# Performance work log

Measured on AMD Instinct MI355X. Metric: run time of the kernel, lower is better.

## Reference

```python
import jax, jax.numpy as jnp
import numpy as np

D_MODEL = 768
N_HEADS = 8
HEAD_DIM = D_MODEL // N_HEADS  # 96


def setup_inputs() -> dict:
    key = jax.random.key(0)
    k1, k2, k3, k4, k5 = jax.random.split(key, 5)
    B, LQ, LK = 2, 4096, 4096
    hidden_states = jax.random.normal(k1, (B, LQ, D_MODEL), dtype=jnp.float32)
    key_value_states = jax.random.normal(k2, (B, LK, D_MODEL), dtype=jnp.float32)
    # learned projection params (initialized as eye in torch, but learned; use random here)
    Wq = jax.random.normal(k3, (D_MODEL, D_MODEL), dtype=jnp.float32) * 0.02
    Wk = jax.random.normal(k4, (D_MODEL, D_MODEL), dtype=jnp.float32) * 0.02
    Wv = jax.random.normal(k5, (D_MODEL, D_MODEL), dtype=jnp.float32) * 0.02
    return {"hidden_states": hidden_states, "key_value_states": key_value_states,
            "Wq": Wq, "Wk": Wk, "Wv": Wv}


def reference(hidden_states, key_value_states, Wq, Wk, Wv):
    B, LQ, _ = hidden_states.shape
    LK = key_value_states.shape[1]
    # linear projections (no bias)
    q = hidden_states @ Wq            # [B, LQ, D]
    k = key_value_states @ Wk         # [B, LK, D]
    v = key_value_states @ Wv         # [B, LK, D]
    # split heads: [B, H, L, d]
    def shape(x, L):
        return x.reshape(B, L, N_HEADS, HEAD_DIM).transpose(0, 2, 1, 3)
    q = shape(q, LQ) / jnp.sqrt(jnp.float32(HEAD_DIM))
    k = shape(k, LK)
    v = shape(v, LK)
    scores = jnp.einsum('bhqd,bhkd->bhqk', q, k)   # [B, H, LQ, LK]
    attn = jax.nn.softmax(scores, axis=-1)
    # dropout p=0.0 -> identity
    ctx = jnp.einsum('bhqk,bhkd->bhqd', attn, v)   # [B, H, LQ, d]
    context = ctx.transpose(0, 2, 1, 3).reshape(B, LQ, D_MODEL)
    return context
```

## Files before the change

kernel.cpp:

```cpp
#include <hip/hip_runtime.h>
#include <hip/hip_bf16.h>


typedef __bf16 bf16x8 __attribute__((ext_vector_type(8)));
typedef __bf16 bf16x4 __attribute__((ext_vector_type(4)));
typedef float  f32x4  __attribute__((ext_vector_type(4)));
typedef float  f32x16 __attribute__((ext_vector_type(16)));
typedef unsigned u32x4 __attribute__((ext_vector_type(4)));

#define DM   768
#define NH   8
#define HD   96
#define SEQ  4096
#define BATCH 2
#define WELEM (DM*DM)
#define XELEM (BATCH*SEQ*DM)

#define GLDS16(gp, lp) __builtin_amdgcn_global_load_lds( \
    (const __attribute__((address_space(1))) void*)(gp), \
    (__attribute__((address_space(3))) void*)(lp), 16, 0, 0)

__global__ __launch_bounds__(256) void prep(
    const float* __restrict__ hidden, const float* __restrict__ kv,
    const float* __restrict__ Wq, const float* __restrict__ Wk,
    const float* __restrict__ Wv,
    __bf16* __restrict__ Xh_bf, __bf16* __restrict__ Xkv_bf,
    __bf16* __restrict__ Tq, __bf16* __restrict__ Tk, __bf16* __restrict__ Tv)
{
    __shared__ __bf16 Ls[64][72];
    const int id = blockIdx.x;
    const int t = threadIdx.x;

    if (id < 6144) {
        const int half = id >= 3072;
        const float* X = half ? kv : hidden;
        __bf16* Y      = half ? Xkv_bf : Xh_bf;
        const size_t i = ((size_t)(id - half * 3072) * 256 + t) * 8;
        float4 lo = *reinterpret_cast<const float4*>(X + i);
        float4 hi = *reinterpret_cast<const float4*>(X + i + 4);
        bf16x8 v;
        v[0]=(__bf16)lo.x; v[1]=(__bf16)lo.y; v[2]=(__bf16)lo.z; v[3]=(__bf16)lo.w;
        v[4]=(__bf16)hi.x; v[5]=(__bf16)hi.y; v[6]=(__bf16)hi.z; v[7]=(__bf16)hi.w;
        *reinterpret_cast<bf16x8*>(Y + i) = v;
        return;
    }

    const int id2 = id - 6144;
    const int which = id2 / 144;
    const int tile = id2 - which * 144;
    const int ti = tile / 12, tj = tile % 12;
    const float* W = (which == 0) ? Wq : (which == 1) ? Wk : Wv;
    __bf16* T      = (which == 0) ? Tq : (which == 1) ? Tk : Tv;

    const int row = t >> 2, q4 = t & 3;
    const float* src = W + (size_t)(ti * 64 + row) * DM + tj * 64 + q4 * 16;
    float4 f0 = *reinterpret_cast<const float4*>(src);
    float4 f1 = *reinterpret_cast<const float4*>(src + 4);
    float4 f2 = *reinterpret_cast<const float4*>(src + 8);
    float4 f3 = *reinterpret_cast<const float4*>(src + 12);
    bf16x8 v0, v1;
    v0[0]=(__bf16)f0.x; v0[1]=(__bf16)f0.y; v0[2]=(__bf16)f0.z; v0[3]=(__bf16)f0.w;
    v0[4]=(__bf16)f1.x; v0[5]=(__bf16)f1.y; v0[6]=(__bf16)f1.z; v0[7]=(__bf16)f1.w;
    v1[0]=(__bf16)f2.x; v1[1]=(__bf16)f2.y; v1[2]=(__bf16)f2.z; v1[3]=(__bf16)f2.w;
    v1[4]=(__bf16)f3.x; v1[5]=(__bf16)f3.y; v1[6]=(__bf16)f3.z; v1[7]=(__bf16)f3.w;
    *reinterpret_cast<bf16x8*>(&Ls[row][q4 * 16])     = v0;
    *reinterpret_cast<bf16x8*>(&Ls[row][q4 * 16 + 8]) = v1;
    __syncthreads();
    #pragma unroll
    for (int j = 0; j < 2; ++j) {
        const int idx = t + j * 256;
        const int orow = idx >> 3, oc = idx & 7;
        bf16x8 o;
        #pragma unroll
        for (int e = 0; e < 8; ++e) o[e] = Ls[oc * 8 + e][orow];
        *reinterpret_cast<bf16x8*>(
            &T[(size_t)(tj * 64 + orow) * DM + ti * 64 + oc * 8]) = o;
    }
}

__global__ __launch_bounds__(256, 2) void proj_all(
    const __bf16* __restrict__ Xh, const __bf16* __restrict__ Xkv,
    const __bf16* __restrict__ Wtq, const __bf16* __restrict__ Wtk,
    const __bf16* __restrict__ Wtv, __bf16* __restrict__ Yq,
    __bf16* __restrict__ Yk, __bf16* __restrict__ Yv, float qscale)
{
    __shared__ __bf16 As[2][128][64];
    __shared__ __bf16 Bs[2][128][64];

    const int t = threadIdx.x;
    const int l = t & 63;
    const int w = t >> 6;
    const int ln = l & 15, g = l >> 4;
    const int wm = w >> 1, wn = w & 1;

    const int id3 = blockIdx.x;
    const int xcd = id3 & 7;
    const int u = id3 >> 3;
    const int which = u % 3;
    const int c = u / 3;
    const int m0 = (xcd * 8 + c / 6) * 128;
    const int n0 = (c % 6) * 128;

    const __bf16* Xb = (which == 0) ? Xh : Xkv;
    const __bf16* Wt = (which == 0) ? Wtq : (which == 1) ? Wtk : Wtv;
    __bf16* Y        = (which == 0) ? Yq : (which == 1) ? Yk : Yv;
    const int mode   = (which == 2) ? 1 : 0;
    const float scale = (which == 0) ? qscale : 1.0f;

    size_t asrc[4], bsrc[4]; unsigned sdst[4];
    #pragma unroll
    for (int j = 0; j < 4; ++j) {
        const int cid = j * 256 + t;
        const int r = cid >> 3, cc = cid & 7, cs = cc ^ (r & 7);
        asrc[j] = (size_t)(m0 + r) * DM + cs * 8;
        bsrc[j] = (size_t)(n0 + r) * DM + cs * 8;
        sdst[j] = cid * 16;
    }

    f32x4 acc[4][4] = {};

    #pragma unroll
    for (int j = 0; j < 4; ++j) GLDS16(Xb + asrc[j], (char*)As + sdst[j]);
    #pragma unroll
    for (int j = 0; j < 4; ++j) GLDS16(Wt + bsrc[j], (char*)Bs + sdst[j]);
    __syncthreads();

    const int NKT = DM / 64;
    for (int kt = 0; kt < NKT; ++kt) {
        const int cur = kt & 1;
        if (kt + 1 < NKT) {
            const unsigned nb = (cur ^ 1) * 16384u;
            const size_t k0n = (size_t)(kt + 1) * 64;
            #pragma unroll
            for (int j = 0; j < 4; ++j) GLDS16(Xb + k0n + asrc[j], (char*)As + nb + sdst[j]);
            #pragma unroll
            for (int j = 0; j < 4; ++j) GLDS16(Wt + k0n + bsrc[j], (char*)Bs + nb + sdst[j]);
        }

        #pragma unroll
        for (int kk = 0; kk < 2; ++kk) {
            bf16x8 a[4], b[4];
            #pragma unroll
            for (int ms = 0; ms < 4; ++ms) {
                const int row = wm * 64 + ms * 16 + ln;
                const int slot = (kk * 4 + g) ^ (row & 7);
                a[ms] = *reinterpret_cast<const bf16x8*>(
                    (const char*)As + cur * 16384 + row * 128 + slot * 16);
            }
            #pragma unroll
            for (int ns = 0; ns < 4; ++ns) {
                const int row = wn * 64 + ns * 16 + ln;
                const int slot = (kk * 4 + g) ^ (row & 7);
                b[ns] = *reinterpret_cast<const bf16x8*>(
                    (const char*)Bs + cur * 16384 + row * 128 + slot * 16);
            }
            #pragma unroll
            for (int ms = 0; ms < 4; ++ms)
                #pragma unroll
                for (int ns = 0; ns < 4; ++ns)
                    acc[ms][ns] = __builtin_amdgcn_mfma_f32_16x16x32_bf16(
                        a[ms], b[ns], acc[ms][ns], 0, 0, 0);
        }
        __syncthreads();
    }

    #pragma unroll
    for (int ms = 0; ms < 4; ++ms) {
        #pragma unroll
        for (int ns = 0; ns < 4; ++ns) {
            const int col = n0 + wn * 64 + ns * 16 + ln;
            const int h = col / HD, d = col - h * HD;
            const int row_base = m0 + wm * 64 + ms * 16 + 4 * g;
            if (mode == 0) {
                #pragma unroll
                for (int r = 0; r < 4; ++r) {
                    const int row = row_base + r;
                    const int b_ = row >> 12, q = row & (SEQ - 1);
                    Y[(((size_t)(b_ * NH + h) * SEQ) + q) * HD + d] =
                        (__bf16)(acc[ms][ns][r] * scale);
                }
            } else {
                const int b_ = row_base >> 12, kq = row_base & (SEQ - 1);
                bf16x4 v;
                #pragma unroll
                for (int r = 0; r < 4; ++r) v[r] = (__bf16)acc[ms][ns][r];
                *reinterpret_cast<bf16x4*>(
                    &Y[((size_t)(b_ * NH + h) * HD + d) * SEQ + kq]) = v;
            }
        }
    }
}

__global__ __launch_bounds__(512, 2) void attn_kernel(
    const __bf16* __restrict__ Q, const __bf16* __restrict__ K,
    const __bf16* __restrict__ Vt, float* __restrict__ out)
{
    __shared__ __bf16 Ks[2][64][128];
    __shared__ __bf16 Vs[2][96][64];

    const int t_ = threadIdx.x;
    const int l = t_ & 63;
    const int w = t_ >> 6;
    const int lh = l >> 5;
    const int c31 = l & 31;
    const int ord = (w >> 2) & 1;

    const int swz = (blockIdx.x & 7) * 32 + (blockIdx.x >> 3);
    const int bh = swz >> 4;
    const int qb = swz & 15;
    const int b = bh >> 3, hd = bh & 7;
    const int q0 = qb * 256 + w * 32;

    const size_t base = (size_t)bh * SEQ * HD;
    const __bf16* Kg = K + base;
    const __bf16* Vg = Vt + base;

    size_t ksrc[2], vsrc[2];
    unsigned kdst[2], vdst[2];
    #pragma unroll
    for (int j = 0; j < 2; ++j) {
        const int cid = j * 512 + t_;
        const int r = cid >> 4, cc = cid & 15;
        int cs = cc ^ (r & 7); if (cs >= 12) cs = 0;
        ksrc[j] = (size_t)r * HD + cs * 8;
        kdst[j] = cid * 16;
        const int vid = j * 512 + t_;
        const int d = vid >> 3, cc2 = vid & 7;
        const int cs2 = cc2 ^ (d & 7);
        vsrc[j] = (size_t)(d < 96 ? d : 0) * SEQ + cs2 * 8;
        vdst[j] = vid * 16;
    }
    const bool vdo2 = t_ < 256;

    bf16x8 qf[6];
    #pragma unroll
    for (int st = 0; st < 6; ++st)
        qf[st] = *reinterpret_cast<const bf16x8*>(
            &Q[base + (size_t)(q0 + c31) * HD + st * 16 + 8 * lh]);

    const char* kb[6];
    #pragma unroll
    for (int st = 0; st < 6; ++st)
        kb[st] = (const char*)Ks + c31 * 256 + (((2 * st + lh) ^ (c31 & 7)) * 16);
    const char* vp[4];
    #pragma unroll
    for (int kc = 0; kc < 4; ++kc)
        vp[kc] = (const char*)Vs + c31 * 128 + (((2 * kc + lh) ^ (c31 & 7)) * 16);

    f32x16 acc[3] = {};
    f32x16 sA0, sA1, sB0, sB1;
    float l_r = 0.f;

    auto STAGE_K = [&](int tile, int kp) {
        const size_t ko = (size_t)tile * 64 * HD;
        #pragma unroll
        for (int j = 0; j < 2; ++j)
            GLDS16(Kg + ko + ksrc[j], (char*)Ks + kp * 16384 + kdst[j]);
    };
    auto STAGE_V = [&](int tile, int vbuf) {
        const size_t vo = (size_t)tile * 64;
        GLDS16(Vg + vo + vsrc[0], (char*)Vs + vbuf * 12288 + vdst[0]);
        if (vdo2)
            GLDS16(Vg + vo + vsrc[1], (char*)Vs + vbuf * 12288 + vdst[1]);
    };

    auto QKT = [&](const int pbuf, f32x16& S0, f32x16& S1) {
        S0 = (f32x16){}; S1 = (f32x16){};
        #pragma unroll
        for (int st = 0; st < 6; ++st) {
            bf16x8 ka0 = *reinterpret_cast<const bf16x8*>(kb[st] + pbuf * 16384);
            bf16x8 ka1 = *reinterpret_cast<const bf16x8*>(kb[st] + pbuf * 16384 + 8192);
            S0 = __builtin_amdgcn_mfma_f32_32x32x16_bf16(ka0, qf[st], S0, 0, 0, 0);
            S1 = __builtin_amdgcn_mfma_f32_32x32x16_bf16(ka1, qf[st], S1, 0, 0, 0);
        }
    };

    auto SMPV = [&](const int vbuf, f32x16& S0, f32x16& S1) {
        float p0 = 0.f, p1 = 0.f;
        #pragma unroll
        for (int r = 0; r < 16; ++r) {
            const float e0 = __builtin_amdgcn_exp2f(S0[r]);
            const float e1 = __builtin_amdgcn_exp2f(S1[r]);
            S0[r] = e0; S1[r] = e1; p0 += e0; p1 += e1;
        }
        l_r += p0 + p1;
        unsigned up[2][4][2];
        #pragma unroll
        for (int qd = 0; qd < 4; ++qd)
            #pragma unroll
            for (int j = 0; j < 2; ++j) {
                asm("v_cvt_pk_bf16_f32 %0, %1, %2"
                    : "=v"(up[0][qd][j])
                    : "v"(S0[4 * qd + 2 * j]), "v"(S0[4 * qd + 2 * j + 1]));
                asm("v_cvt_pk_bf16_f32 %0, %1, %2"
                    : "=v"(up[1][qd][j])
                    : "v"(S1[4 * qd + 2 * j]), "v"(S1[4 * qd + 2 * j + 1]));
            }
        #pragma unroll
        for (int kc = 0; kc < 4; ++kc) {
            const int ks = kc >> 1, cp = kc & 1;
            unsigned x0 = up[ks][2 * cp][0],     x1 = up[ks][2 * cp][1];
            unsigned y0 = up[ks][2 * cp + 1][0], y1 = up[ks][2 * cp + 1][1];
            asm("v_permlane32_swap_b32 %0, %1" : "+v"(x0), "+v"(y0));
            asm("v_permlane32_swap_b32 %0, %1" : "+v"(x1), "+v"(y1));
            u32x4 pw; pw[0] = x0; pw[1] = x1; pw[2] = y0; pw[3] = y1;
            const bf16x8 pa = __builtin_bit_cast(bf16x8, pw);
            __builtin_amdgcn_s_setprio(1);
            #pragma unroll
            for (int dt = 0; dt < 3; ++dt) {
                bf16x8 vb = *reinterpret_cast<const bf16x8*>(
                    vp[kc] + vbuf * 12288 + dt * 4096);
                acc[dt] = __builtin_amdgcn_mfma_f32_32x32x16_bf16(pa, vb, acc[dt], 0, 0, 0);
            }
            __builtin_amdgcn_s_setprio(0);
        }
    };

    STAGE_K(0, 0);
    STAGE_V(0, 0);
    __syncthreads();
    STAGE_K(1, 1);
    QKT(0, sA0, sA1);

    const int NT = SEQ / 64;
    if (ord == 0) {
        for (int u2 = 0; u2 < NT / 2; ++u2) {
            const int u = 2 * u2;
            __syncthreads();
            if (u + 2 < NT) STAGE_K(u + 2, 0);
            STAGE_V(u + 1, 1);
            QKT(1, sB0, sB1);
            SMPV(0, sA0, sA1);
            __syncthreads();
            if (u + 3 < NT) STAGE_K(u + 3, 1);
            if (u + 2 < NT) STAGE_V(u + 2, 0);
            if (u + 2 < NT) QKT(0, sA0, sA1);
            SMPV(1, sB0, sB1);
        }
    } else {
        for (int u2 = 0; u2 < NT / 2; ++u2) {
            const int u = 2 * u2;
            __syncthreads();
            if (u + 2 < NT) STAGE_K(u + 2, 0);
            STAGE_V(u + 1, 1);
            SMPV(0, sA0, sA1);
            QKT(1, sB0, sB1);
            __syncthreads();
            if (u + 3 < NT) STAGE_K(u + 3, 1);
            if (u + 2 < NT) STAGE_V(u + 2, 0);
            SMPV(1, sB0, sB1);
            if (u + 2 < NT) QKT(0, sA0, sA1);
        }
    }

    {
        float ex = l_r;
        asm volatile("" : "+v"(ex));
        asm("v_permlane32_swap_b32 %0, %1" : "+v"(ex), "+v"(l_r));
        l_r += ex;
    }
    const float inv = 1.0f / l_r;
    #pragma unroll
    for (int r = 0; r < 16; ++r) {
        const int ql = (r & 3) + 8 * (r >> 2) + 4 * lh;
        const float ir = __shfl(inv, ql, 64);
        const int q = q0 + ql;
        float* dst = out + ((size_t)(b * SEQ + q)) * DM + hd * HD;
        #pragma unroll
        for (int dt = 0; dt < 3; ++dt)
            dst[dt * 32 + c31] = acc[dt][r] * ir;
    }
}

extern "C" void kernel_launch(void* const* d_in, const int* in_sizes, int n_in,
                              void* d_out, int out_size, void* d_ws, size_t ws_size,
                              hipStream_t stream) {
    const float* hidden = (const float*)d_in[0];
    const float* kv     = (const float*)d_in[1];
    const float* Wq     = (const float*)d_in[2];
    const float* Wk     = (const float*)d_in[3];
    const float* Wv     = (const float*)d_in[4];
    float* out = (float*)d_out;

    __bf16* Wt_q = (__bf16*)d_ws;
    __bf16* Wt_k = Wt_q + WELEM;
    __bf16* Wt_v = Wt_k + WELEM;
    __bf16* Qb   = Wt_v + WELEM;
    __bf16* Kb   = Qb + XELEM;
    __bf16* Vtb  = Kb + XELEM;

    __bf16* Xh_bf  = (__bf16*)d_out;
    __bf16* Xkv_bf = Xh_bf + XELEM;

    prep<<<6576, 256, 0, stream>>>(hidden, kv, Wq, Wk, Wv,
                                   Xh_bf, Xkv_bf, Wt_q, Wt_k, Wt_v);

    const float qscale = 0.10206207261596575f * 1.4426950408889634f;
    proj_all<<<1152, 256, 0, stream>>>(Xh_bf, Xkv_bf, Wt_q, Wt_k, Wt_v,
                                       Qb, Kb, Vtb, qscale);

    attn_kernel<<<256, 512, 0, stream>>>(Qb, Kb, Vtb, out);
}
```

Baseline: 169.5 us.

## Split attention over key halves and combine partial results in a second kernel

The attention kernel now splits the key sequence into two halves, and each block handles 512 queries (64 per wave, two 32-row MFMA tiles) against one 2048-key half. K and V tiles shrink to 32 keys, so each K fragment read from LDS feeds two MFMAs. Each block writes unnormalized fp32 partial contexts and row sums to the output or a scratch buffer. A new combine kernel adds the two partials and divides by the summed row totals. This raises register use and LDS reuse per wave, at the cost of writing and re-reading a full fp32 context buffer plus an extra launch. The softmax has no running max, so adding the two unnormalized halves stays exact.

```diff
diff --git a/kernel.cpp b/kernel.cpp
--- a/kernel.cpp
+++ b/kernel.cpp
@@ -191,12 +191,13 @@
     }
 }
 
-__global__ __launch_bounds__(512, 2) void attn_kernel(
+__global__ __launch_bounds__(512, 2) void attn_split(
     const __bf16* __restrict__ Q, const __bf16* __restrict__ K,
-    const __bf16* __restrict__ Vt, float* __restrict__ out)
+    const __bf16* __restrict__ Vt, float* __restrict__ ctx0,
+    float* __restrict__ ctx1, float* __restrict__ lsum)
 {
-    __shared__ __bf16 Ks[2][64][128];
-    __shared__ __bf16 Vs[2][96][64];
+    __shared__ __bf16 Ks[2][32][128];
+    __shared__ __bf16 Vs[2][96][32];
 
     const int t_ = threadIdx.x;
     const int l = t_ & 63;
@@ -207,71 +208,63 @@
 
     const int swz = (blockIdx.x & 7) * 32 + (blockIdx.x >> 3);
     const int bh = swz >> 4;
-    const int qb = swz & 15;
+    const int rem = swz & 15;
+    const int kh = rem >> 3;
+    const int qbb = rem & 7;
     const int b = bh >> 3, hd = bh & 7;
-    const int q0 = qb * 256 + w * 32;
+    const int q0 = qbb * 512 + w * 64;
 
     const size_t base = (size_t)bh * SEQ * HD;
-    const __bf16* Kg = K + base;
-    const __bf16* Vg = Vt + base;
-
-    size_t ksrc[2], vsrc[2];
-    unsigned kdst[2], vdst[2];
-    #pragma unroll
-    for (int j = 0; j < 2; ++j) {
-        const int cid = j * 512 + t_;
-        const int r = cid >> 4, cc = cid & 15;
-        int cs = cc ^ (r & 7); if (cs >= 12) cs = 0;
-        ksrc[j] = (size_t)r * HD + cs * 8;
-        kdst[j] = cid * 16;
-        const int vid = j * 512 + t_;
-        const int d = vid >> 3, cc2 = vid & 7;
-        const int cs2 = cc2 ^ (d & 7);
-        vsrc[j] = (size_t)(d < 96 ? d : 0) * SEQ + cs2 * 8;
-        vdst[j] = vid * 16;
-    }
-    const bool vdo2 = t_ < 256;
-
-    bf16x8 qf[6];
-    #pragma unroll
-    for (int st = 0; st < 6; ++st)
-        qf[st] = *reinterpret_cast<const bf16x8*>(
-            &Q[base + (size_t)(q0 + c31) * HD + st * 16 + 8 * lh]);
+    const __bf16* Kg = K + base + (size_t)kh * 2048 * HD;
+    const __bf16* Vg = Vt + base + (size_t)kh * 2048;
+
+    const int kr = t_ >> 4, kcc = t_ & 15;
+    int kcs = kcc ^ (kr & 7); if (kcs >= 12) kcs = 0;
+    const size_t ksrc = (size_t)kr * HD + kcs * 8;
+    const unsigned kdst = t_ * 16;
+    const int vd = t_ >> 2, vcc = t_ & 3;
+    const int vcs = (vcc - (vd >> 1)) & 3;
+    const size_t vsrc = (size_t)(vd < 96 ? vd : 0) * SEQ + vcs * 8;
+    const unsigned vdst = t_ * 16;
+    const bool vdo = t_ < 384;
+
+    bf16x8 qf[2][6];
+    #pragma unroll
+    for (int qh = 0; qh < 2; ++qh)
+        #pragma unroll
+        for (int st = 0; st < 6; ++st)
+            qf[qh][st] = *reinterpret_cast<const bf16x8*>(
+                &Q[base + (size_t)(q0 + qh * 32 + c31) * HD + st * 16 + 8 * lh]);
 
     const char* kb[6];
     #pragma unroll
     for (int st = 0; st < 6; ++st)
         kb[st] = (const char*)Ks + c31 * 256 + (((2 * st + lh) ^ (c31 & 7)) * 16);
-    const char* vp[4];
-    #pragma unroll
-    for (int kc = 0; kc < 4; ++kc)
-        vp[kc] = (const char*)Vs + c31 * 128 + (((2 * kc + lh) ^ (c31 & 7)) * 16);
-
-    f32x16 acc[3] = {};
+    const char* vp[2];
+    #pragma unroll
+    for (int kc = 0; kc < 2; ++kc)
+        vp[kc] = (const char*)Vs + c31 * 64 +
+                 (((2 * kc + lh + (c31 >> 1)) & 3) * 16);
+
+    f32x16 acc[2][3] = {};
     f32x16 sA0, sA1, sB0, sB1;
-    float l_r = 0.f;
+    float l_r[2] = {0.f, 0.f};
 
     auto STAGE_K = [&](int tile, int kp) {
-        const size_t ko = (size_t)tile * 64 * HD;
-        #pragma unroll
-        for (int j = 0; j < 2; ++j)
-            GLDS16(Kg + ko + ksrc[j], (char*)Ks + kp * 16384 + kdst[j]);
+        GLDS16(Kg + (size_t)tile * 32 * HD + ksrc, (char*)Ks + kp * 8192 + kdst);
     };
     auto STAGE_V = [&](int tile, int vbuf) {
-        const size_t vo = (size_t)tile * 64;
-        GLDS16(Vg + vo + vsrc[0], (char*)Vs + vbuf * 12288 + vdst[0]);
-        if (vdo2)
-            GLDS16(Vg + vo + vsrc[1], (char*)Vs + vbuf * 12288 + vdst[1]);
+        if (vdo)
+            GLDS16(Vg + (size_t)tile * 32 + vsrc, (char*)Vs + vbuf * 6144 + vdst);
     };
 
     auto QKT = [&](const int pbuf, f32x16& S0, f32x16& S1) {
         S0 = (f32x16){}; S1 = (f32x16){};
         #pragma unroll
         for (int st = 0; st < 6; ++st) {
-            bf16x8 ka0 = *reinterpret_cast<const bf16x8*>(kb[st] + pbuf * 16384);
-            bf16x8 ka1 = *reinterpret_cast<const bf16x8*>(kb[st] + pbuf * 16384 + 8192);
-            S0 = __builtin_amdgcn_mfma_f32_32x32x16_bf16(ka0, qf[st], S0, 0, 0, 0);
-            S1 = __builtin_amdgcn_mfma_f32_32x32x16_bf16(ka1, qf[st], S1, 0, 0, 0);
+            bf16x8 ka = *reinterpret_cast<const bf16x8*>(kb[st] + pbuf * 8192);
+            S0 = __builtin_amdgcn_mfma_f32_32x32x16_bf16(ka, qf[0][st], S0, 0, 0, 0);
+            S1 = __builtin_amdgcn_mfma_f32_32x32x16_bf16(ka, qf[1][st], S1, 0, 0, 0);
         }
     };
 
@@ -283,7 +276,7 @@
             const float e1 = __builtin_amdgcn_exp2f(S1[r]);
             S0[r] = e0; S1[r] = e1; p0 += e0; p1 += e1;
         }
-        l_r += p0 + p1;
+        l_r[0] += p0; l_r[1] += p1;
         unsigned up[2][4][2];
         #pragma unroll
         for (int qd = 0; qd < 4; ++qd)
@@ -297,20 +290,24 @@
                     : "v"(S1[4 * qd + 2 * j]), "v"(S1[4 * qd + 2 * j + 1]));
             }
         #pragma unroll
-        for (int kc = 0; kc < 4; ++kc) {
-            const int ks = kc >> 1, cp = kc & 1;
-            unsigned x0 = up[ks][2 * cp][0],     x1 = up[ks][2 * cp][1];
-            unsigned y0 = up[ks][2 * cp + 1][0], y1 = up[ks][2 * cp + 1][1];
-            asm("v_permlane32_swap_b32 %0, %1" : "+v"(x0), "+v"(y0));
-            asm("v_permlane32_swap_b32 %0, %1" : "+v"(x1), "+v"(y1));
-            u32x4 pw; pw[0] = x0; pw[1] = x1; pw[2] = y0; pw[3] = y1;
-            const bf16x8 pa = __builtin_bit_cast(bf16x8, pw);
+        for (int kc = 0; kc < 2; ++kc) {
+            bf16x8 pa[2];
+            #pragma unroll
+            for (int qh = 0; qh < 2; ++qh) {
+                unsigned x0 = up[qh][2 * kc][0],     x1 = up[qh][2 * kc][1];
+                unsigned y0 = up[qh][2 * kc + 1][0], y1 = up[qh][2 * kc + 1][1];
+                asm("v_permlane32_swap_b32 %0, %1" : "+v"(x0), "+v"(y0));
+                asm("v_permlane32_swap_b32 %0, %1" : "+v"(x1), "+v"(y1));
+                u32x4 pw; pw[0] = x0; pw[1] = x1; pw[2] = y0; pw[3] = y1;
+                pa[qh] = __builtin_bit_cast(bf16x8, pw);
+            }
             __builtin_amdgcn_s_setprio(1);
             #pragma unroll
             for (int dt = 0; dt < 3; ++dt) {
                 bf16x8 vb = *reinterpret_cast<const bf16x8*>(
-                    vp[kc] + vbuf * 12288 + dt * 4096);
-                acc[dt] = __builtin_amdgcn_mfma_f32_32x32x16_bf16(pa, vb, acc[dt], 0, 0, 0);
+                    vp[kc] + vbuf * 6144 + dt * 2048);
+                acc[0][dt] = __builtin_amdgcn_mfma_f32_32x32x16_bf16(pa[0], vb, acc[0][dt], 0, 0, 0);
+                acc[1][dt] = __builtin_amdgcn_mfma_f32_32x32x16_bf16(pa[1], vb, acc[1][dt], 0, 0, 0);
             }
             __builtin_amdgcn_s_setprio(0);
         }
@@ -322,7 +319,7 @@
     STAGE_K(1, 1);
     QKT(0, sA0, sA1);
 
-    const int NT = SEQ / 64;
+    const int NT = 2048 / 32;
     if (ord == 0) {
         for (int u2 = 0; u2 < NT / 2; ++u2) {
             const int u = 2 * u2;
@@ -353,23 +350,49 @@
         }
     }
 
-    {
-        float ex = l_r;
+    #pragma unroll
+    for (int qh = 0; qh < 2; ++qh) {
+        float ex = l_r[qh];
         asm volatile("" : "+v"(ex));
-        asm("v_permlane32_swap_b32 %0, %1" : "+v"(ex), "+v"(l_r));
-        l_r += ex;
-    }
-    const float inv = 1.0f / l_r;
-    #pragma unroll
-    for (int r = 0; r < 16; ++r) {
-        const int ql = (r & 3) + 8 * (r >> 2) + 4 * lh;
-        const float ir = __shfl(inv, ql, 64);
-        const int q = q0 + ql;
-        float* dst = out + ((size_t)(b * SEQ + q)) * DM + hd * HD;
-        #pragma unroll
-        for (int dt = 0; dt < 3; ++dt)
-            dst[dt * 32 + c31] = acc[dt][r] * ir;
-    }
+        asm("v_permlane32_swap_b32 %0, %1" : "+v"(ex), "+v"(l_r[qh]));
+        l_r[qh] += ex;
+    }
+    float* ctx = kh ? ctx1 : ctx0;
+    #pragma unroll
+    for (int qh = 0; qh < 2; ++qh) {
+        #pragma unroll
+        for (int r = 0; r < 16; ++r) {
+            const int ql = (r & 3) + 8 * (r >> 2) + 4 * lh;
+            const int q = q0 + qh * 32 + ql;
+            float* dst = ctx + ((size_t)(b * SEQ + q)) * DM + hd * HD;
+            #pragma unroll
+            for (int dt = 0; dt < 3; ++dt)
+                dst[dt * 32 + c31] = acc[qh][dt][r];
+        }
+        if (lh == 0)
+            lsum[kh * 65536 + bh * SEQ + q0 + qh * 32 + c31] = l_r[qh];
+    }
+}
+
+__global__ __launch_bounds__(256) void combine2(
+    const float* __restrict__ ctx1, const float* __restrict__ lsum,
+    float* __restrict__ outc)
+{
+    const size_t e4 = (size_t)blockIdx.x * 256 + threadIdx.x;
+    const size_t e = e4 * 4;
+    const int row = (int)(e / DM);
+    const int dfull = (int)(e - (size_t)row * DM);
+    const int hd = dfull / HD;
+    const int b = row >> 12, q = row & (SEQ - 1);
+    const int bh = b * NH + hd;
+    const float lv = lsum[bh * SEQ + q] + lsum[65536 + bh * SEQ + q];
+    const float inv = 1.0f / lv;
+    float4 c0 = *reinterpret_cast<const float4*>(outc + e);
+    float4 c1 = *reinterpret_cast<const float4*>(ctx1 + e);
+    float4 o;
+    o.x = (c0.x + c1.x) * inv; o.y = (c0.y + c1.y) * inv;
+    o.z = (c0.z + c1.z) * inv; o.w = (c0.w + c1.w) * inv;
+    *reinterpret_cast<float4*>(outc + e) = o;
 }
 
 extern "C" void kernel_launch(void* const* d_in, const int* in_sizes, int n_in,
@@ -388,6 +411,8 @@
     __bf16* Qb   = Wt_v + WELEM;
     __bf16* Kb   = Qb + XELEM;
     __bf16* Vtb  = Kb + XELEM;
+    float*  ctx1 = (float*)(Vtb + XELEM);
+    float*  lsum = ctx1 + XELEM;
 
     __bf16* Xh_bf  = (__bf16*)d_out;
     __bf16* Xkv_bf = Xh_bf + XELEM;
@@ -399,5 +424,6 @@
     proj_all<<<1152, 256, 0, stream>>>(Xh_bf, Xkv_bf, Wt_q, Wt_k, Wt_v,
                                        Qb, Kb, Vtb, qscale);
 
-    attn_kernel<<<256, 512, 0, stream>>>(Qb, Kb, Vtb, out);
+    attn_split<<<256, 512, 0, stream>>>(Qb, Kb, Vtb, out, ctx1, lsum);
+    combine2<<<XELEM / 4 / 256, 256, 0, stream>>>(ctx1, lsum, out);
 }
```

Measured after the change: 181.2 us. 1.07x slower.
